# Optimization experiments

Hardware: AMD Instinct MI355X
Metric: run time of the kernel (lower is better)

Reference implementation:

```python
import jax, jax.numpy as jnp
import numpy as np
from jax import lax

N_FFT = 16
HOP = 4
WIN_LEN = 16
OUT_WINDOW = 128  # adaptive pool output size
B, L, C = 32, 4096, 64
OUT_FEATURE = 512


def _stft_mag(x_bcl):
    # x_bcl: [B, C, L] float32. Replicates torch.stft(center=True, reflect pad,
    # periodic hann window, onesided) followed by abs().
    win = 0.5 * (1.0 - jnp.cos(2.0 * jnp.pi * jnp.arange(WIN_LEN) / WIN_LEN))  # periodic hann
    pad = N_FFT // 2
    xp = jnp.pad(x_bcl, ((0, 0), (0, 0), (pad, pad)), mode='reflect')
    T = 1 + x_bcl.shape[-1] // HOP  # centered frame count
    idx = np.arange(T)[:, None] * HOP + np.arange(N_FFT)[None, :]  # [T, n_fft] static
    frames = xp[..., idx]                       # [B, C, T, n_fft]
    spec = jnp.fft.rfft(frames * win, axis=-1)  # [B, C, T, F], F = n_fft//2+1
    return jnp.abs(spec).transpose(0, 1, 3, 2)  # [B, C, F, T]


def _adaptive_avg_pool1d(x_nct, out_size):
    # Matches torch adaptive_avg_pool1d: bin i covers [floor(i*N/out), ceil((i+1)*N/out))
    N = x_nct.shape[-1]
    starts = (np.arange(out_size) * N) // out_size
    ends = -((-(np.arange(out_size) + 1) * N) // out_size)  # ceil div
    csum = jnp.concatenate(
        [jnp.zeros(x_nct.shape[:-1] + (1,), x_nct.dtype), jnp.cumsum(x_nct, axis=-1)], axis=-1)
    sums = csum[..., ends] - csum[..., starts]
    counts = jnp.asarray(ends - starts, x_nct.dtype)
    return sums / counts


def setup_inputs() -> dict:
    key = jax.random.key(0)
    k1, k2, k3 = jax.random.split(key, 3)
    in_ch = C * (N_FFT // 2 + 1)  # 576
    x = jax.random.normal(k1, (B, L, C), dtype=jnp.float32)
    fan_in = in_ch * 3
    bound = 1.0 / np.sqrt(fan_in)
    weight = jax.random.uniform(k2, (OUT_FEATURE, in_ch, 3), jnp.float32, -bound, bound)
    bias = jax.random.uniform(k3, (OUT_FEATURE,), jnp.float32, -bound, bound)
    return {"x": x, "weight": weight, "bias": bias}


def reference(x, weight, bias):
    # x: [B, L, C]
    mags = _stft_mag(x.transpose(0, 2, 1))            # [B, C, F, T]
    Bb, Cc, F, T = mags.shape
    m = mags.reshape(Bb, Cc * F, T)                    # [B, C*F, T]
    y = lax.conv_general_dilated(
        m, weight, window_strides=(1,), padding='VALID',
        dimension_numbers=('NCH', 'OIH', 'NCH'))       # [B, out_feature, T-2]
    y = y + bias[None, :, None]
    y = _adaptive_avg_pool1d(y, OUT_WINDOW)            # [B, out_feature, window]
    return y.transpose(0, 2, 1)                        # [B, window, out_feature]
```

## Files before the change

### kernel.cpp

```cpp
#include <hip/hip_runtime.h>
#include <hip/hip_bf16.h>

#define BATCH 32
#define LTOT 4096
#define CCH 64
#define NFFT 16
#define HOP 4
#define NF 9
#define T_FR 1025
#define ICH 576
#define OCH 512
#define TY 1023
#define OUTW 128
#define KTOT 1728

typedef __attribute__((ext_vector_type(8))) _Float16 half8;
typedef __attribute__((ext_vector_type(4))) float floatx4;

__device__ constexpr float C16[16] = {
    1.0f,  0.923879533f,  0.707106781f,  0.382683432f,  0.0f, -0.382683432f,
   -0.707106781f, -0.923879533f, -1.0f, -0.923879533f, -0.707106781f,
   -0.382683432f,  0.0f,  0.382683432f,  0.707106781f,  0.923879533f};

#define C1F 0.923879533f
#define C2F 0.707106781f
#define C3F 0.382683432f

__device__ __forceinline__ void async_copy16(const _Float16* g, _Float16* l) {
  __builtin_amdgcn_global_load_lds(
      (const __attribute__((address_space(1))) unsigned int*)g,
      (__attribute__((address_space(3))) unsigned int*)l, 16, 0, 0);
}

__device__ __forceinline__ float fsqrt_fast(float v) {
  float r;
  asm("v_sqrt_f32 %0, %1" : "=v"(r) : "v"(v));
  return r;
}

__global__ __launch_bounds__(256) void stft_pool_kernel(
    const float* __restrict__ x, const float* __restrict__ weight,
    _Float16* __restrict__ pm, _Float16* __restrict__ wkr) {
  const int w = blockIdx.x, b = blockIdx.y;
  const int tid = threadIdx.x;

  const int gid = (b * 128 + w) * 256 + tid;
  if (gid < OCH * ICH) {
    int o = gid / ICH, i = gid - o * ICH;
    int c = i / 9, f = i - c * 9;
    const float* src = weight + (size_t)o * (ICH * 3) + i * 3;
    _Float16* dst = wkr + (size_t)o * KTOT + f * 64 + c;
#pragma unroll
    for (int k = 0; k < 3; ++k)
      dst[k * ICH] = (_Float16)src[k];
  }

  const int s = (w * TY) >> 7;
  const int e = ((w + 1) * TY + 127) >> 7;
  const int cnt = e - s;
  const int R = cnt + 2;
  const float inv = 1.0f / (float)cnt;

  __shared__ float arena[56 * 64];
  float* xs = arena;
  float* red = arena;

  const int l_base = s * 4 - 8;
  const int nrow = R * 4 + 12;
  const float* xb = x + (size_t)b * LTOT * CCH;
#pragma unroll
  for (int it = 0; it < 4; ++it) {
    int u = it * 256 + tid;
    int r = u >> 4, c4 = u & 15;
    if (r < nrow) {
      int l = l_base + r;
      if (l < 0) l = -l;
      if (l >= LTOT) l = 2 * LTOT - 2 - l;
      *(floatx4*)(&xs[r * 64 + c4 * 4]) =
          *(const floatx4*)(&xb[(size_t)l * CCH + c4 * 4]);
    }
  }
  __syncthreads();

  const int c = tid & 63, tq = tid >> 6;

  float acc[3][NF];
#pragma unroll
  for (int k = 0; k < 3; ++k)
#pragma unroll
    for (int f = 0; f < NF; ++f) acc[k][f] = 0.0f;

#pragma unroll
  for (int it = 0; it < 3; ++it) {
    const int rl = tq + it * 4;
    if (rl < R) {
      float wx[16];
#pragma unroll
      for (int j = 0; j < 16; ++j)
        wx[j] = xs[(rl * 4 + j) * 64 + c] * (0.5f * (1.0f - C16[j]));
      const float s1 = wx[1] + wx[15], d1 = wx[1] - wx[15];
      const float s2 = wx[2] + wx[14], d2 = wx[2] - wx[14];
      const float s3 = wx[3] + wx[13], d3 = wx[3] - wx[13];
      const float s4 = wx[4] + wx[12], d4 = wx[4] - wx[12];
      const float s5 = wx[5] + wx[11], d5 = wx[5] - wx[11];
      const float s6 = wx[6] + wx[10], d6 = wx[6] - wx[10];
      const float s7 = wx[7] + wx[9],  d7 = wx[7] - wx[9];
      const float wxp = wx[0] + wx[8], wxm = wx[0] - wx[8];
      const float u1 = s2 - s6, u2 = s1 - s7, u3 = s3 - s5;
      const float v1 = d2 + d6, v2 = d1 + d7, v3 = d3 + d5;
      const float Se = s2 + s4 + s6;
      const float So = (s1 + s3) + (s5 + s7);
      const float re0 = wxp + Se + So;
      const float re8 = wxp + (Se - So);
      const float tA = C2F * u1;
      const float A1 = wxm + tA, A3 = wxm - tA;
      const float B1 = C1F * u2 + C3F * u3;
      const float B3 = C3F * u2 - C1F * u3;
      const float tP = C2F * v1;
      const float P1 = d4 + tP, P3 = tP - d4;
      const float Q1 = C3F * v2 + C1F * v3;
      const float Q3 = C1F * v2 - C3F * v3;
      const float A2 = wxp - s4;
      const float B2 = C2F * (((s1 - s3) - s5) + s7);
      const float P2 = d2 - d6;
      const float Q2 = C2F * (((d1 + d3) - d5) - d7);
      const float re4 = ((wxp - s2) + s4) - s6;
      const float im4 = ((d1 - d3) + d5) - d7;

      float mg[NF];
      mg[0] = (float)(_Float16)fabsf(re0);
      mg[8] = (float)(_Float16)fabsf(re8);
      {
        const float r1 = A1 + B1, i1 = P1 + Q1;
        mg[1] = (float)(_Float16)fsqrt_fast(r1 * r1 + i1 * i1);
        const float r7 = A1 - B1, i7 = Q1 - P1;
        mg[7] = (float)(_Float16)fsqrt_fast(r7 * r7 + i7 * i7);
        const float r2 = A2 + B2, i2 = P2 + Q2;
        mg[2] = (float)(_Float16)fsqrt_fast(r2 * r2 + i2 * i2);
        const float r6 = A2 - B2, i6 = Q2 - P2;
        mg[6] = (float)(_Float16)fsqrt_fast(r6 * r6 + i6 * i6);
        const float r3 = A3 + B3, i3 = P3 + Q3;
        mg[3] = (float)(_Float16)fsqrt_fast(r3 * r3 + i3 * i3);
        const float r5 = A3 - B3, i5 = Q3 - P3;
        mg[5] = (float)(_Float16)fsqrt_fast(r5 * r5 + i5 * i5);
        mg[4] = (float)(_Float16)fsqrt_fast(re4 * re4 + im4 * im4);
      }
#pragma unroll
      for (int k = 0; k < 3; ++k)
        if ((unsigned)(rl - k) < (unsigned)cnt)
#pragma unroll
          for (int f = 0; f < NF; ++f) acc[k][f] += mg[f];
    }
  }

  __syncthreads();

  if (tq < 2) {
#pragma unroll
    for (int k = 0; k < 3; ++k)
#pragma unroll
      for (int f = 0; f < NF; ++f)
        red[((tq * 27) + k * 9 + f) * 64 + c] = acc[k][f];
  }
  __syncthreads();
  if (tq >= 2) {
#pragma unroll
    for (int k = 0; k < 3; ++k)
#pragma unroll
      for (int f = 0; f < NF; ++f) {
        const int idx = (((tq - 2) * 27) + k * 9 + f) * 64 + c;
        red[idx] += acc[k][f];
      }
  }
  __syncthreads();

  _Float16* pmo = pm + ((size_t)b * OUTW + w) * KTOT;
  for (int j = tid; j < KTOT; j += 256) {
    const int k = j / ICH;
    const int rem = j - k * ICH;
    const int f = rem >> 6;
    const int cc = rem & 63;
    const int base = (k * 9 + f) * 64 + cc;
    const float sum = red[base] + red[27 * 64 + base];
    pmo[j] = (_Float16)(sum * inv);
  }
}

__global__ __launch_bounds__(256, 2) void gemm_pooled_kernel(
    const _Float16* __restrict__ pm, const _Float16* __restrict__ wkr,
    const float* __restrict__ bias, float* __restrict__ out) {
  const int lid = blockIdx.x;
  const int xcd = lid & 7;
  const int rest = lid >> 3;
  const int m8 = rest & 7;
  const int bq = rest >> 3;
  const int b = bq * 8 + xcd;
  const int o0 = m8 * 64;

  const int tid = threadIdx.x;
  const int wave = tid >> 6, lane = tid & 63;
  const int wm = wave >> 1, wn = wave & 1;

  __shared__ _Float16 as[64 * 64];
  __shared__ _Float16 bs[128 * 64];

  floatx4 acc[2][4];
#pragma unroll
  for (int mt = 0; mt < 2; ++mt)
#pragma unroll
    for (int nt = 0; nt < 4; ++nt)
      acc[mt][nt] = (floatx4)0.0f;

  const int frow = lane & 15;
  const int quad = lane >> 4;
  const int l7 = lane & 7;
  const int srow = lane >> 3;
  const int ssrc_off = srow * KTOT + (l7 ^ srow) * 8;

  const _Float16* ab = wkr + (size_t)o0 * KTOT;
  const _Float16* bb = pm + (size_t)b * OUTW * KTOT;

  for (int kb = 0; kb < 27; ++kb) {
    const int i0 = kb * 64;
#pragma unroll
    for (int it = 0; it < 2; ++it) {
      const int seg = wave * 2 + it;
      async_copy16(ab + (size_t)(seg * 8) * KTOT + i0 + ssrc_off,
                   &as[seg * 512]);
    }
#pragma unroll
    for (int it = 0; it < 4; ++it) {
      const int seg = wave * 4 + it;
      async_copy16(bb + (size_t)(seg * 8) * KTOT + i0 + ssrc_off,
                   &bs[seg * 512]);
    }
    __syncthreads();

#pragma unroll
    for (int kk2 = 0; kk2 < 2; ++kk2) {
      const int jj = kk2 * 4 + quad;
      const int coff = ((jj ^ l7) << 3);
      half8 af[2], bf[4];
#pragma unroll
      for (int mt = 0; mt < 2; ++mt)
        af[mt] = *(const half8*)(&as[(wm * 32 + mt * 16 + frow) * 64 + coff]);
#pragma unroll
      for (int nt = 0; nt < 4; ++nt)
        bf[nt] = *(const half8*)(&bs[(wn * 64 + nt * 16 + frow) * 64 + coff]);
#pragma unroll
      for (int mt = 0; mt < 2; ++mt)
#pragma unroll
        for (int nt = 0; nt < 4; ++nt)
          acc[mt][nt] = __builtin_amdgcn_mfma_f32_16x16x32_f16(
              bf[nt], af[mt], acc[mt][nt], 0, 0, 0);
    }
    __syncthreads();
  }

  const int col = lane & 15;
  float* ob = out + (size_t)b * OUTW * OCH;
#pragma unroll
  for (int nt = 0; nt < 4; ++nt) {
    const int wb = wn * 64 + nt * 16 + quad * 4;
#pragma unroll
    for (int r = 0; r < 4; ++r) {
      const int w = wb + r;
#pragma unroll
      for (int mt = 0; mt < 2; ++mt) {
        const int o = o0 + wm * 32 + mt * 16 + col;
        ob[(size_t)w * OCH + o] = bias[o] + acc[mt][nt][r];
      }
    }
  }
}

extern "C" void kernel_launch(void* const* d_in, const int* in_sizes, int n_in,
                              void* d_out, int out_size, void* d_ws, size_t ws_size,
                              hipStream_t stream) {
  const float* x = (const float*)d_in[0];
  const float* weight = (const float*)d_in[1];
  const float* bias = (const float*)d_in[2];
  float* out = (float*)d_out;

  char* ws = (char*)d_ws;
  const size_t w_bytes = (size_t)OCH * KTOT * sizeof(_Float16);
  _Float16* wkr = (_Float16*)ws;
  _Float16* pm = (_Float16*)(ws + w_bytes);

  hipLaunchKernelGGL(stft_pool_kernel, dim3(OUTW, BATCH), dim3(256), 0,
                     stream, x, weight, pm, wkr);
  hipLaunchKernelGGL(gemm_pooled_kernel, dim3(256), dim3(256), 0, stream,
                     pm, wkr, bias, out);
}
```

Before: 114.4 us.

## Double-buffer GEMM LDS tiles with async prefetch and drop fp16 magnitude rounding

The pooled GEMM now keeps two LDS buffers for the A and B tiles. It issues the async global-to-LDS loads for the next K block before computing the current one, then waits with a partial vmcnt and a raw s_barrier, so memory latency can overlap the MFMA work. Separately, the STFT kernel stops rounding each magnitude through fp16 before accumulating, which removes some conversion instructions and slightly changes numerics. Doubling the LDS footprint may lower occupancy, and the hand-written waitcnt and barrier carry a risk of ordering mistakes.

Result: no change. 112.6 us (median of 2 runs) (-1.6%).

```diff
diff --git a/kernel.cpp b/kernel.cpp
--- a/kernel.cpp
+++ b/kernel.cpp
@@ -37,6 +37,9 @@
   asm("v_sqrt_f32 %0, %1" : "=v"(r) : "v"(v));
   return r;
 }
+
+#define SBAR() asm volatile("s_barrier" ::: "memory")
+#define WAITV(N) asm volatile("s_waitcnt vmcnt(" #N ")" ::: "memory")
 
 __global__ __launch_bounds__(256) void stft_pool_kernel(
     const float* __restrict__ x, const float* __restrict__ weight,
@@ -128,22 +131,22 @@
       const float im4 = ((d1 - d3) + d5) - d7;
 
       float mg[NF];
-      mg[0] = (float)(_Float16)fabsf(re0);
-      mg[8] = (float)(_Float16)fabsf(re8);
+      mg[0] = fabsf(re0);
+      mg[8] = fabsf(re8);
       {
         const float r1 = A1 + B1, i1 = P1 + Q1;
-        mg[1] = (float)(_Float16)fsqrt_fast(r1 * r1 + i1 * i1);
+        mg[1] = fsqrt_fast(r1 * r1 + i1 * i1);
         const float r7 = A1 - B1, i7 = Q1 - P1;
-        mg[7] = (float)(_Float16)fsqrt_fast(r7 * r7 + i7 * i7);
+        mg[7] = fsqrt_fast(r7 * r7 + i7 * i7);
         const float r2 = A2 + B2, i2 = P2 + Q2;
-        mg[2] = (float)(_Float16)fsqrt_fast(r2 * r2 + i2 * i2);
+        mg[2] = fsqrt_fast(r2 * r2 + i2 * i2);
         const float r6 = A2 - B2, i6 = Q2 - P2;
-        mg[6] = (float)(_Float16)fsqrt_fast(r6 * r6 + i6 * i6);
+        mg[6] = fsqrt_fast(r6 * r6 + i6 * i6);
         const float r3 = A3 + B3, i3 = P3 + Q3;
-        mg[3] = (float)(_Float16)fsqrt_fast(r3 * r3 + i3 * i3);
+        mg[3] = fsqrt_fast(r3 * r3 + i3 * i3);
         const float r5 = A3 - B3, i5 = Q3 - P3;
-        mg[5] = (float)(_Float16)fsqrt_fast(r5 * r5 + i5 * i5);
-        mg[4] = (float)(_Float16)fsqrt_fast(re4 * re4 + im4 * im4);
+        mg[5] = fsqrt_fast(r5 * r5 + i5 * i5);
+        mg[4] = fsqrt_fast(re4 * re4 + im4 * im4);
       }
 #pragma unroll
       for (int k = 0; k < 3; ++k)
@@ -201,8 +204,8 @@
   const int wave = tid >> 6, lane = tid & 63;
   const int wm = wave >> 1, wn = wave & 1;
 
-  __shared__ _Float16 as[64 * 64];
-  __shared__ _Float16 bs[128 * 64];
+  __shared__ _Float16 as[2][64 * 64];
+  __shared__ _Float16 bs[2][128 * 64];
 
   floatx4 acc[2][4];
 #pragma unroll
@@ -220,21 +223,31 @@
   const _Float16* ab = wkr + (size_t)o0 * KTOT;
   const _Float16* bb = pm + (size_t)b * OUTW * KTOT;
 
+#define GSTAGE(kbx, buf)                                                     \
+  {                                                                          \
+    const int i0s = (kbx) * 64;                                              \
+    _Pragma("unroll") for (int it = 0; it < 2; ++it) {                       \
+      const int seg = wave * 2 + it;                                         \
+      async_copy16(ab + (size_t)(seg * 8) * KTOT + i0s + ssrc_off,           \
+                   &as[buf][seg * 512]);                                     \
+    }                                                                        \
+    _Pragma("unroll") for (int it = 0; it < 4; ++it) {                       \
+      const int seg = wave * 4 + it;                                         \
+      async_copy16(bb + (size_t)(seg * 8) * KTOT + i0s + ssrc_off,           \
+                   &bs[buf][seg * 512]);                                     \
+    }                                                                        \
+  }
+
+  GSTAGE(0, 0);
   for (int kb = 0; kb < 27; ++kb) {
-    const int i0 = kb * 64;
-#pragma unroll
-    for (int it = 0; it < 2; ++it) {
-      const int seg = wave * 2 + it;
-      async_copy16(ab + (size_t)(seg * 8) * KTOT + i0 + ssrc_off,
-                   &as[seg * 512]);
-    }
-#pragma unroll
-    for (int it = 0; it < 4; ++it) {
-      const int seg = wave * 4 + it;
-      async_copy16(bb + (size_t)(seg * 8) * KTOT + i0 + ssrc_off,
-                   &bs[seg * 512]);
-    }
-    __syncthreads();
+    const int cur = kb & 1;
+    if (kb < 26) {
+      GSTAGE(kb + 1, cur ^ 1);
+      WAITV(6);
+    } else {
+      WAITV(0);
+    }
+    SBAR();
 
 #pragma unroll
     for (int kk2 = 0; kk2 < 2; ++kk2) {
@@ -243,10 +256,12 @@
       half8 af[2], bf[4];
 #pragma unroll
       for (int mt = 0; mt < 2; ++mt)
-        af[mt] = *(const half8*)(&as[(wm * 32 + mt * 16 + frow) * 64 + coff]);
+        af[mt] =
+            *(const half8*)(&as[cur][(wm * 32 + mt * 16 + frow) * 64 + coff]);
 #pragma unroll
       for (int nt = 0; nt < 4; ++nt)
-        bf[nt] = *(const half8*)(&bs[(wn * 64 + nt * 16 + frow) * 64 + coff]);
+        bf[nt] =
+            *(const half8*)(&bs[cur][(wn * 64 + nt * 16 + frow) * 64 + coff]);
 #pragma unroll
       for (int mt = 0; mt < 2; ++mt)
 #pragma unroll
@@ -254,7 +269,7 @@
           acc[mt][nt] = __builtin_amdgcn_mfma_f32_16x16x32_f16(
               bf[nt], af[mt], acc[mt][nt], 0, 0, 0);
     }
-    __syncthreads();
+    SBAR();
   }
 
   const int col = lane & 15;
```
